# Kernel optimization log

Measured on AMD Instinct MI355X. Metric: run time of the kernel, lower is better.

The kernel has to match this reference:

```python
import jax, jax.numpy as jnp
import numpy as np

N, C_IN, C_HID, C_OUT = 50000, 256, 64 * 4, 64
E = 1_600_000
P_DROP = 0.5


def setup_inputs() -> dict:
    key = jax.random.key(0)
    ks = jax.random.split(key, 12)
    cat = C_IN + C_HID  # DConv input is concat([X, H]) -> in+hidden channels
    glorot = lambda k, sh: jax.random.normal(k, sh, jnp.float32) * (2.0 / (sh[-2] + sh[-1])) ** 0.5
    inp = {
        "x": jax.random.normal(ks[0], (N, C_IN), jnp.float32),
        "edge_index": jax.random.randint(ks[1], (2, E), 0, N, jnp.int64),
        "edge_weight": jax.random.uniform(ks[2], (E,), jnp.float32),
        # deterministic dropout mask (training-mode dropout, p=0.5), pre-scaled by 1/(1-p)
        "mask": (jax.random.uniform(ks[3], (N, C_IN)) >= P_DROP).astype(jnp.float32) / (1.0 - P_DROP),
        # DConv weights: shape (2, K=1, in+hidden, hidden) per gate
        "w_z": glorot(ks[4], (2, 1, cat, C_HID)),
        "b_z": jnp.zeros((C_HID,), jnp.float32),
        "w_r": glorot(ks[5], (2, 1, cat, C_HID)),
        "b_r": jnp.zeros((C_HID,), jnp.float32),
        "w_h": glorot(ks[6], (2, 1, cat, C_HID)),
        "b_h": jnp.zeros((C_HID,), jnp.float32),
        "w_lin": glorot(ks[7], (C_OUT, C_HID)),
        "b_lin": jnp.zeros((C_OUT,), jnp.float32),
    }
    return inp


def _dconv(inp, w, b):
    # K=1 diffusion conv: only the zeroth-order (identity) term of both the
    # forward- and backward-transition expansions survives; edges are unused.
    return inp @ w[0, 0] + inp @ w[1, 0] + b


def reference(x, edge_index, edge_weight, mask, w_z, b_z, w_r, b_r, w_h, b_h, w_lin, b_lin):
    x = x * mask  # F.dropout, training=True, deterministic mask
    H = jnp.zeros((x.shape[0], w_z.shape[-1]), x.dtype)  # initial hidden state
    xh = jnp.concatenate([x, H], axis=1)                  # [N, in+hid]
    Z = jax.nn.sigmoid(_dconv(xh, w_z, b_z))              # update gate
    R = jax.nn.sigmoid(_dconv(xh, w_r, b_r))              # reset gate
    xhr = jnp.concatenate([x, H * R], axis=1)
    H_tilde = jnp.tanh(_dconv(xhr, w_h, b_h))             # candidate state
    H = Z * H + (1.0 - Z) * H_tilde                       # GRU blend
    h = jax.nn.elu(H)
    return h @ w_lin.T + b_lin                            # [N, out]
```

## Files before the change

kernel.cpp:

```cpp
#include <hip/hip_runtime.h>
#include <hip/hip_bf16.h>


typedef __attribute__((ext_vector_type(8))) short bf16x8;
typedef __attribute__((ext_vector_type(4))) float f32x4;

constexpr int N_ROWS = 50000;
constexpr int CIN  = 256;
constexpr int COUT = 64;
constexpr int BM   = 32;

__device__ inline unsigned short f2bf(float f) {
    union { float f; unsigned u; } v; v.f = f;
    unsigned r = v.u + 0x7fffu + ((v.u >> 16) & 1u);
    return (unsigned short)(r >> 16);
}
__device__ inline float bf2f(unsigned short b) {
    union { unsigned u; float f; } v; v.u = ((unsigned)b) << 16;
    return v.f;
}
__device__ inline f32x4 mfma16(bf16x8 a, bf16x8 b, f32x4 c) {
    return __builtin_amdgcn_mfma_f32_16x16x32_bf16(a, b, c, 0, 0, 0);
}

__global__ __launch_bounds__(256) void prep_frags(
    const float* __restrict__ wz, const float* __restrict__ wh,
    const float* __restrict__ wlin, unsigned short* __restrict__ ws)
{
    int t = blockIdx.x * 256 + threadIdx.x;
    int frag = t >> 6, lane = t & 63;
    if (frag >= 288) return;
    int g16 = lane & 15, kg = lane >> 4;
    unsigned short vals[8];
    if (frag < 256) {
        int kb = frag & 7, nf = (frag >> 3) & 15, g = frag >> 7;
        const float* wsrc = g ? wh : wz;
        int n = nf * 16 + g16;
        #pragma unroll
        for (int j = 0; j < 8; ++j) {
            int k = kb * 32 + kg * 8 + j;
            float v = wsrc[k * 256 + n] + wsrc[131072 + k * 256 + n];
            vals[j] = f2bf(v);
        }
    } else {
        int f = frag - 256;
        int kb = f & 7, nf = f >> 3;
        int n = nf * 16 + g16;
        #pragma unroll
        for (int j = 0; j < 8; ++j) {
            int k = kb * 32 + kg * 8 + j;
            vals[j] = f2bf(wlin[n * 256 + k]);
        }
    }
    unsigned short* dst = ws + (size_t)frag * 512 + lane * 8;
    #pragma unroll
    for (int j = 0; j < 8; ++j) dst[j] = vals[j];
}

__device__ inline bf16x8 ldfrag(const unsigned short* wf, int frag, int lane) {
    return *reinterpret_cast<const bf16x8*>(wf + (size_t)frag * 512 + lane * 8);
}

__global__ __launch_bounds__(256, 3) void dcrnn_mfma(
    const float* __restrict__ x, const float* __restrict__ mask,
    const unsigned short* __restrict__ wf,
    const float* __restrict__ bz, const float* __restrict__ bh,
    const float* __restrict__ blin, float* __restrict__ out)
{
    __shared__ char smem[32768];
    char* AhiB = smem;
    char* AloB = smem + 16384;
    const int tid = threadIdx.x, lane = tid & 63, wv = tid >> 6;
    const int l16 = lane & 15, lk = lane >> 4;
    const int row0 = blockIdx.x * BM;
    const int nfg0 = wv * 4;

    bf16x8 cZ = ldfrag(wf, (nfg0)      * 8, lane);
    bf16x8 cH = ldfrag(wf, (16 + nfg0) * 8, lane);

    #pragma unroll
    for (int it = 0; it < 8; ++it) {
        int f = it * 256 + tid;
        int r = f >> 6, c4 = f & 63;
        int row = row0 + r;
        float4 xv = make_float4(0.f, 0.f, 0.f, 0.f), mv = xv;
        if (row < N_ROWS) {
            xv = reinterpret_cast<const float4*>(x    + (size_t)row * CIN)[c4];
            mv = reinterpret_cast<const float4*>(mask + (size_t)row * CIN)[c4];
        }
        float v0 = xv.x * mv.x, v1 = xv.y * mv.y, v2 = xv.z * mv.z, v3 = xv.w * mv.w;
        unsigned short h0 = f2bf(v0), h1 = f2bf(v1), h2 = f2bf(v2), h3 = f2bf(v3);
        unsigned short l0 = f2bf(v0 - bf2f(h0)), l1 = f2bf(v1 - bf2f(h1));
        unsigned short l2 = f2bf(v2 - bf2f(h2)), l3 = f2bf(v3 - bf2f(h3));
        int byte = ((r * CIN + c4 * 4) * 2) ^ ((r & 7) << 4);
        *reinterpret_cast<ushort4*>(AhiB + byte) = make_ushort4(h0, h1, h2, h3);
        *reinterpret_cast<ushort4*>(AloB + byte) = make_ushort4(l0, l1, l2, l3);
    }
    __syncthreads();

    f32x4 accZ[2][4], accH[2][4];
    #pragma unroll
    for (int m = 0; m < 2; ++m)
        #pragma unroll
        for (int nf = 0; nf < 4; ++nf) {
            accZ[m][nf] = (f32x4){0.f, 0.f, 0.f, 0.f};
            accH[m][nf] = (f32x4){0.f, 0.f, 0.f, 0.f};
        }

    bf16x8 ah[2], al[2];
    {
        int koff = lk * 8;
        #pragma unroll
        for (int m = 0; m < 2; ++m) {
            int row = m * 16 + l16;
            int byte = ((row * CIN + koff) * 2) ^ ((row & 7) << 4);
            ah[m] = *reinterpret_cast<const bf16x8*>(AhiB + byte);
            al[m] = *reinterpret_cast<const bf16x8*>(AloB + byte);
        }
    }

    for (int kb = 0; kb < 8; ++kb) {
        #pragma unroll
        for (int nf = 0; nf < 4; ++nf) {
            int nnf = (nf + 1) & 3;
            int nkb = kb + (nf == 3 ? 1 : 0);
            int nkbc = nkb > 7 ? 7 : nkb;
            bf16x8 nZ = ldfrag(wf, (nfg0 + nnf)      * 8 + nkbc, lane);
            bf16x8 nH = ldfrag(wf, (16 + nfg0 + nnf) * 8 + nkbc, lane);
            #pragma unroll
            for (int m = 0; m < 2; ++m) {
                accZ[m][nf] = mfma16(ah[m], cZ, accZ[m][nf]);
                accZ[m][nf] = mfma16(al[m], cZ, accZ[m][nf]);
                accH[m][nf] = mfma16(ah[m], cH, accH[m][nf]);
                accH[m][nf] = mfma16(al[m], cH, accH[m][nf]);
            }
            if (nf == 3) {
                int akb = kb < 7 ? kb + 1 : 7;
                int koff = akb * 32 + lk * 8;
                #pragma unroll
                for (int m = 0; m < 2; ++m) {
                    int row = m * 16 + l16;
                    int byte = ((row * CIN + koff) * 2) ^ ((row & 7) << 4);
                    ah[m] = *reinterpret_cast<const bf16x8*>(AhiB + byte);
                    al[m] = *reinterpret_cast<const bf16x8*>(AloB + byte);
                }
            }
            cZ = nZ; cH = nH;
        }
    }
    __syncthreads();

    #pragma unroll
    for (int nf = 0; nf < 4; ++nf) {
        int col = wv * 64 + nf * 16 + l16;
        float bzv = bz[col], bhv = bh[col];
        #pragma unroll
        for (int m = 0; m < 2; ++m) {
            #pragma unroll
            for (int i = 0; i < 4; ++i) {
                float z  = 1.f / (1.f + __expf(-(accZ[m][nf][i] + bzv)));
                float t  = __expf(2.f * (accH[m][nf][i] + bhv));
                float th = (t - 1.f) / (t + 1.f);
                float H  = (1.f - z) * th;
                float h  = (H > 0.f) ? H : (__expf(H) - 1.f);
                int row = m * 16 + lk * 4 + i;
                unsigned pk = ((unsigned)f2bf(h)) << 16;
                int byte = (row * 1024 + col * 4) ^ ((row & 7) << 4);
                *reinterpret_cast<unsigned*>(smem + byte) = pk;
            }
        }
    }
    __syncthreads();

    f32x4 accO[2];
    #pragma unroll
    for (int m = 0; m < 2; ++m) accO[m] = (f32x4){0.f, 0.f, 0.f, 0.f};

    bf16x8 cb = ldfrag(wf, 256 + wv * 8, lane);
    for (int kb = 0; kb < 8; ++kb) {
        int nk = kb < 7 ? kb + 1 : 7;
        bf16x8 nb = ldfrag(wf, 256 + wv * 8 + nk, lane);
        #pragma unroll
        for (int m = 0; m < 2; ++m) {
            int row = m * 16 + l16;
            int e0  = kb * 32 + lk * 8;
            int b0  = (row * 1024 + e0 * 4)      ^ ((row & 7) << 4);
            int b1  = (row * 1024 + e0 * 4 + 16) ^ ((row & 7) << 4);
            uint4 p0 = *reinterpret_cast<const uint4*>(smem + b0);
            uint4 p1 = *reinterpret_cast<const uint4*>(smem + b1);
            bf16x8 ha;
            ha[0] = (short)(p0.x >> 16); ha[1] = (short)(p0.y >> 16);
            ha[2] = (short)(p0.z >> 16); ha[3] = (short)(p0.w >> 16);
            ha[4] = (short)(p1.x >> 16); ha[5] = (short)(p1.y >> 16);
            ha[6] = (short)(p1.z >> 16); ha[7] = (short)(p1.w >> 16);
            accO[m] = mfma16(ha, cb, accO[m]);
        }
        cb = nb;
    }
    {
        int col = wv * 16 + l16;
        float bo = blin[col];
        #pragma unroll
        for (int m = 0; m < 2; ++m)
            #pragma unroll
            for (int i = 0; i < 4; ++i) {
                int row = row0 + m * 16 + lk * 4 + i;
                if (row < N_ROWS) out[(size_t)row * COUT + col] = accO[m][i] + bo;
            }
    }
}

__global__ __launch_bounds__(256) void fallback_f32(
    const float* __restrict__ x, const float* __restrict__ mask,
    const float* __restrict__ wzr, const float* __restrict__ whr,
    const float* __restrict__ bz, const float* __restrict__ bh,
    const float* __restrict__ wlinr, const float* __restrict__ blin,
    float* __restrict__ out)
{
    __shared__ float xm[32][CIN];
    const int tid = threadIdx.x;
    const int row0 = blockIdx.x * 32;
    #pragma unroll
    for (int it = 0; it < 8; ++it) {
        int idx = it * 256 + tid;
        int r = idx >> 6, c4 = idx & 63, row = row0 + r;
        float4 v = make_float4(0.f, 0.f, 0.f, 0.f);
        if (row < N_ROWS) {
            float4 a = reinterpret_cast<const float4*>(x    + (size_t)row * CIN)[c4];
            float4 m = reinterpret_cast<const float4*>(mask + (size_t)row * CIN)[c4];
            v = make_float4(a.x * m.x, a.y * m.y, a.z * m.z, a.w * m.w);
        }
        reinterpret_cast<float4*>(&xm[r][0])[c4] = v;
    }
    __syncthreads();
    const int j0 = (tid & 63) * 4, r0 = (tid >> 6) * 8;
    float accz[4][8], acch[4][8];
    #pragma unroll
    for (int c = 0; c < 4; ++c)
        #pragma unroll
        for (int r = 0; r < 8; ++r) { accz[c][r] = 0.f; acch[c][r] = 0.f; }
    for (int k = 0; k < CIN; k += 4) {
        float4 wz4[4], wh4[4];
        #pragma unroll
        for (int kk = 0; kk < 4; ++kk) {
            float4 a0 = *reinterpret_cast<const float4*>(&wzr[(k + kk) * 256 + j0]);
            float4 a1 = *reinterpret_cast<const float4*>(&wzr[131072 + (k + kk) * 256 + j0]);
            wz4[kk] = make_float4(a0.x + a1.x, a0.y + a1.y, a0.z + a1.z, a0.w + a1.w);
            float4 b0 = *reinterpret_cast<const float4*>(&whr[(k + kk) * 256 + j0]);
            float4 b1 = *reinterpret_cast<const float4*>(&whr[131072 + (k + kk) * 256 + j0]);
            wh4[kk] = make_float4(b0.x + b1.x, b0.y + b1.y, b0.z + b1.z, b0.w + b1.w);
        }
        #pragma unroll
        for (int r = 0; r < 8; ++r) {
            float4 xv = *reinterpret_cast<const float4*>(&xm[r0 + r][k]);
            float xk[4] = {xv.x, xv.y, xv.z, xv.w};
            float wzc[4][4] = {{wz4[0].x,wz4[0].y,wz4[0].z,wz4[0].w},{wz4[1].x,wz4[1].y,wz4[1].z,wz4[1].w},
                               {wz4[2].x,wz4[2].y,wz4[2].z,wz4[2].w},{wz4[3].x,wz4[3].y,wz4[3].z,wz4[3].w}};
            float whc[4][4] = {{wh4[0].x,wh4[0].y,wh4[0].z,wh4[0].w},{wh4[1].x,wh4[1].y,wh4[1].z,wh4[1].w},
                               {wh4[2].x,wh4[2].y,wh4[2].z,wh4[2].w},{wh4[3].x,wh4[3].y,wh4[3].z,wh4[3].w}};
            #pragma unroll
            for (int kk = 0; kk < 4; ++kk)
                #pragma unroll
                for (int c = 0; c < 4; ++c) {
                    accz[c][r] = fmaf(xk[kk], wzc[kk][c], accz[c][r]);
                    acch[c][r] = fmaf(xk[kk], whc[kk][c], acch[c][r]);
                }
        }
    }
    float bzj[4], bhj[4];
    #pragma unroll
    for (int c = 0; c < 4; ++c) { bzj[c] = bz[j0 + c]; bhj[c] = bh[j0 + c]; }
    __syncthreads();
    #pragma unroll
    for (int r = 0; r < 8; ++r) {
        float hc[4];
        #pragma unroll
        for (int c = 0; c < 4; ++c) {
            float z  = 1.f / (1.f + expf(-(accz[c][r] + bzj[c])));
            float ht = tanhf(acch[c][r] + bhj[c]);
            float H  = (1.f - z) * ht;
            hc[c] = (H > 0.f) ? H : expm1f(H);
        }
        *reinterpret_cast<float4*>(&xm[r0 + r][j0]) = make_float4(hc[0], hc[1], hc[2], hc[3]);
    }
    __syncthreads();
    const int o = tid & 63;
    float acc[8];
    #pragma unroll
    for (int r = 0; r < 8; ++r) acc[r] = 0.f;
    for (int k = 0; k < CIN; k += 4) {
        float4 wv4 = *reinterpret_cast<const float4*>(&wlinr[o * 256 + k]);
        #pragma unroll
        for (int r = 0; r < 8; ++r) {
            float4 hv = *reinterpret_cast<const float4*>(&xm[r0 + r][k]);
            acc[r] = fmaf(hv.x, wv4.x, acc[r]);
            acc[r] = fmaf(hv.y, wv4.y, acc[r]);
            acc[r] = fmaf(hv.z, wv4.z, acc[r]);
            acc[r] = fmaf(hv.w, wv4.w, acc[r]);
        }
    }
    float bo = blin[o];
    #pragma unroll
    for (int r = 0; r < 8; ++r) {
        int row = row0 + r0 + r;
        if (row < N_ROWS) out[(size_t)row * COUT + o] = acc[r] + bo;
    }
}

extern "C" void kernel_launch(void* const* d_in, const int* in_sizes, int n_in,
                              void* d_out, int out_size, void* d_ws, size_t ws_size,
                              hipStream_t stream)
{
    const float* x    = (const float*)d_in[0];
    const float* mask = (const float*)d_in[3];
    const float* wz   = (const float*)d_in[4];
    const float* bz   = (const float*)d_in[5];
    const float* wh   = (const float*)d_in[8];
    const float* bh   = (const float*)d_in[9];
    const float* wlin = (const float*)d_in[10];
    const float* blin = (const float*)d_in[11];
    float* outf = (float*)d_out;

    const size_t ws_need = 288 * 1024;
    if (ws_size >= ws_need) {
        unsigned short* wsf = (unsigned short*)d_ws;
        prep_frags<<<72, 256, 0, stream>>>(wz, wh, wlin, wsf);
        dcrnn_mfma<<<(N_ROWS + BM - 1) / BM, 256, 0, stream>>>(
            x, mask, wsf, bz, bh, blin, outf);
    } else {
        fallback_f32<<<(N_ROWS + 31) / 32, 256, 0, stream>>>(
            x, mask, wz, wh, bz, bh, wlin, blin, outf);
    }
}
```

Measured before the change: 64.31 us.

## Use 512-thread blocks splitting gate columns and output rows across eight waves

Doubles the block to eight waves, so each wave computes two 16-column gate fragments instead of four, and in the output GEMM each wave handles one 16-row by 16-column tile. This halves per-wave accumulator registers and MFMA work and spreads the 32-row tile over more waves to raise parallelism and latency hiding. The cost is that A fragments are now reloaded from LDS every k-block by twice as many waves, which adds LDS traffic, and each wave has less work to amortise its fixed overhead.

```diff
diff --git a/kernel.cpp b/kernel.cpp
--- a/kernel.cpp
+++ b/kernel.cpp
@@ -61,7 +61,7 @@
     return *reinterpret_cast<const bf16x8*>(wf + (size_t)frag * 512 + lane * 8);
 }
 
-__global__ __launch_bounds__(256, 3) void dcrnn_mfma(
+__global__ __launch_bounds__(512, 4) void dcrnn_mfma(
     const float* __restrict__ x, const float* __restrict__ mask,
     const unsigned short* __restrict__ wf,
     const float* __restrict__ bz, const float* __restrict__ bh,
@@ -73,14 +73,17 @@
     const int tid = threadIdx.x, lane = tid & 63, wv = tid >> 6;
     const int l16 = lane & 15, lk = lane >> 4;
     const int row0 = blockIdx.x * BM;
-    const int nfg0 = wv * 4;
-
-    bf16x8 cZ = ldfrag(wf, (nfg0)      * 8, lane);
-    bf16x8 cH = ldfrag(wf, (16 + nfg0) * 8, lane);
-
-    #pragma unroll
-    for (int it = 0; it < 8; ++it) {
-        int f = it * 256 + tid;
+    const int nf0 = wv * 2;
+
+    bf16x8 rZ[2], rH[2];
+    rZ[0] = ldfrag(wf, (nf0 + 0)      * 8, lane);
+    rH[0] = ldfrag(wf, (16 + nf0 + 0) * 8, lane);
+    rZ[1] = ldfrag(wf, (nf0 + 1)      * 8, lane);
+    rH[1] = ldfrag(wf, (16 + nf0 + 1) * 8, lane);
+
+    #pragma unroll
+    for (int it = 0; it < 4; ++it) {
+        int f = it * 512 + tid;
         int r = f >> 6, c4 = f & 63;
         int row = row0 + r;
         float4 xv = make_float4(0.f, 0.f, 0.f, 0.f), mv = xv;
@@ -98,18 +101,18 @@
     }
     __syncthreads();
 
-    f32x4 accZ[2][4], accH[2][4];
-    #pragma unroll
-    for (int m = 0; m < 2; ++m)
-        #pragma unroll
-        for (int nf = 0; nf < 4; ++nf) {
-            accZ[m][nf] = (f32x4){0.f, 0.f, 0.f, 0.f};
-            accH[m][nf] = (f32x4){0.f, 0.f, 0.f, 0.f};
-        }
-
-    bf16x8 ah[2], al[2];
-    {
-        int koff = lk * 8;
+    f32x4 accZ[2][2], accH[2][2];
+    #pragma unroll
+    for (int nfi = 0; nfi < 2; ++nfi)
+        #pragma unroll
+        for (int m = 0; m < 2; ++m) {
+            accZ[nfi][m] = (f32x4){0.f, 0.f, 0.f, 0.f};
+            accH[nfi][m] = (f32x4){0.f, 0.f, 0.f, 0.f};
+        }
+
+    for (int kb = 0; kb < 8; ++kb) {
+        bf16x8 ah[2], al[2];
+        int koff = kb * 32 + lk * 8;
         #pragma unroll
         for (int m = 0; m < 2; ++m) {
             int row = m * 16 + l16;
@@ -117,49 +120,36 @@
             ah[m] = *reinterpret_cast<const bf16x8*>(AhiB + byte);
             al[m] = *reinterpret_cast<const bf16x8*>(AloB + byte);
         }
-    }
-
-    for (int kb = 0; kb < 8; ++kb) {
-        #pragma unroll
-        for (int nf = 0; nf < 4; ++nf) {
-            int nnf = (nf + 1) & 3;
-            int nkb = kb + (nf == 3 ? 1 : 0);
-            int nkbc = nkb > 7 ? 7 : nkb;
-            bf16x8 nZ = ldfrag(wf, (nfg0 + nnf)      * 8 + nkbc, lane);
-            bf16x8 nH = ldfrag(wf, (16 + nfg0 + nnf) * 8 + nkbc, lane);
+        #pragma unroll
+        for (int nfi = 0; nfi < 2; ++nfi) {
+            int nkb = kb < 7 ? kb + 1 : 7;
+            bf16x8 nZ = ldfrag(wf, (nf0 + nfi)      * 8 + nkb, lane);
+            bf16x8 nH = ldfrag(wf, (16 + nf0 + nfi) * 8 + nkb, lane);
             #pragma unroll
             for (int m = 0; m < 2; ++m) {
-                accZ[m][nf] = mfma16(ah[m], cZ, accZ[m][nf]);
-                accZ[m][nf] = mfma16(al[m], cZ, accZ[m][nf]);
-                accH[m][nf] = mfma16(ah[m], cH, accH[m][nf]);
-                accH[m][nf] = mfma16(al[m], cH, accH[m][nf]);
+                accZ[nfi][m] = mfma16(ah[m], rZ[nfi], accZ[nfi][m]);
+                accZ[nfi][m] = mfma16(al[m], rZ[nfi], accZ[nfi][m]);
+                accH[nfi][m] = mfma16(ah[m], rH[nfi], accH[nfi][m]);
+                accH[nfi][m] = mfma16(al[m], rH[nfi], accH[nfi][m]);
             }
-            if (nf == 3) {
-                int akb = kb < 7 ? kb + 1 : 7;
-                int koff = akb * 32 + lk * 8;
-                #pragma unroll
-                for (int m = 0; m < 2; ++m) {
-                    int row = m * 16 + l16;
-                    int byte = ((row * CIN + koff) * 2) ^ ((row & 7) << 4);
-                    ah[m] = *reinterpret_cast<const bf16x8*>(AhiB + byte);
-                    al[m] = *reinterpret_cast<const bf16x8*>(AloB + byte);
-                }
-            }
-            cZ = nZ; cH = nH;
-        }
-    }
-    __syncthreads();
-
-    #pragma unroll
-    for (int nf = 0; nf < 4; ++nf) {
-        int col = wv * 64 + nf * 16 + l16;
+            rZ[nfi] = nZ; rH[nfi] = nH;
+        }
+    }
+
+    bf16x8 cb = ldfrag(wf, 256 + (wv & 3) * 8, lane);
+
+    __syncthreads();
+
+    #pragma unroll
+    for (int nfi = 0; nfi < 2; ++nfi) {
+        int col = wv * 32 + nfi * 16 + l16;
         float bzv = bz[col], bhv = bh[col];
         #pragma unroll
         for (int m = 0; m < 2; ++m) {
             #pragma unroll
             for (int i = 0; i < 4; ++i) {
-                float z  = 1.f / (1.f + __expf(-(accZ[m][nf][i] + bzv)));
-                float t  = __expf(2.f * (accH[m][nf][i] + bhv));
+                float z  = 1.f / (1.f + __expf(-(accZ[nfi][m][i] + bzv)));
+                float t  = __expf(2.f * (accH[nfi][m][i] + bhv));
                 float th = (t - 1.f) / (t + 1.f);
                 float H  = (1.f - z) * th;
                 float h  = (H > 0.f) ? H : (__expf(H) - 1.f);
@@ -172,41 +162,33 @@
     }
     __syncthreads();
 
-    f32x4 accO[2];
-    #pragma unroll
-    for (int m = 0; m < 2; ++m) accO[m] = (f32x4){0.f, 0.f, 0.f, 0.f};
-
-    bf16x8 cb = ldfrag(wf, 256 + wv * 8, lane);
+    f32x4 accO = (f32x4){0.f, 0.f, 0.f, 0.f};
+    const int mo = wv >> 2;
     for (int kb = 0; kb < 8; ++kb) {
         int nk = kb < 7 ? kb + 1 : 7;
-        bf16x8 nb = ldfrag(wf, 256 + wv * 8 + nk, lane);
-        #pragma unroll
-        for (int m = 0; m < 2; ++m) {
-            int row = m * 16 + l16;
-            int e0  = kb * 32 + lk * 8;
-            int b0  = (row * 1024 + e0 * 4)      ^ ((row & 7) << 4);
-            int b1  = (row * 1024 + e0 * 4 + 16) ^ ((row & 7) << 4);
-            uint4 p0 = *reinterpret_cast<const uint4*>(smem + b0);
-            uint4 p1 = *reinterpret_cast<const uint4*>(smem + b1);
-            bf16x8 ha;
-            ha[0] = (short)(p0.x >> 16); ha[1] = (short)(p0.y >> 16);
-            ha[2] = (short)(p0.z >> 16); ha[3] = (short)(p0.w >> 16);
-            ha[4] = (short)(p1.x >> 16); ha[5] = (short)(p1.y >> 16);
-            ha[6] = (short)(p1.z >> 16); ha[7] = (short)(p1.w >> 16);
-            accO[m] = mfma16(ha, cb, accO[m]);
-        }
+        bf16x8 nb = ldfrag(wf, 256 + (wv & 3) * 8 + nk, lane);
+        int row = mo * 16 + l16;
+        int e0  = kb * 32 + lk * 8;
+        int b0  = (row * 1024 + e0 * 4)      ^ ((row & 7) << 4);
+        int b1  = (row * 1024 + e0 * 4 + 16) ^ ((row & 7) << 4);
+        uint4 p0 = *reinterpret_cast<const uint4*>(smem + b0);
+        uint4 p1 = *reinterpret_cast<const uint4*>(smem + b1);
+        bf16x8 ha;
+        ha[0] = (short)(p0.x >> 16); ha[1] = (short)(p0.y >> 16);
+        ha[2] = (short)(p0.z >> 16); ha[3] = (short)(p0.w >> 16);
+        ha[4] = (short)(p1.x >> 16); ha[5] = (short)(p1.y >> 16);
+        ha[6] = (short)(p1.z >> 16); ha[7] = (short)(p1.w >> 16);
+        accO = mfma16(ha, cb, accO);
         cb = nb;
     }
     {
-        int col = wv * 16 + l16;
+        int col = (wv & 3) * 16 + l16;
         float bo = blin[col];
         #pragma unroll
-        for (int m = 0; m < 2; ++m)
-            #pragma unroll
-            for (int i = 0; i < 4; ++i) {
-                int row = row0 + m * 16 + lk * 4 + i;
-                if (row < N_ROWS) out[(size_t)row * COUT + col] = accO[m][i] + bo;
-            }
+        for (int i = 0; i < 4; ++i) {
+            int row = row0 + mo * 16 + lk * 4 + i;
+            if (row < N_ROWS) out[(size_t)row * COUT + col] = accO[i] + bo;
+        }
     }
 }
 
@@ -325,7 +307,7 @@
     if (ws_size >= ws_need) {
         unsigned short* wsf = (unsigned short*)d_ws;
         prep_frags<<<72, 256, 0, stream>>>(wz, wh, wlin, wsf);
-        dcrnn_mfma<<<(N_ROWS + BM - 1) / BM, 256, 0, stream>>>(
+        dcrnn_mfma<<<(N_ROWS + BM - 1) / BM, 512, 0, stream>>>(
             x, mask, wsf, bz, bh, blin, outf);
     } else {
         fallback_f32<<<(N_ROWS + 31) / 32, 256, 0, stream>>>(
```

Measured after the change: 62.69 us. 2.5% less time.
